# Kernel tuning notes

Measured on AMD Instinct MI355X. Metric: run time of the kernel, lower is better.

## Reference

```python
import jax, jax.numpy as jnp
import numpy as np

B, H, S, D = 4, 16, 2048, 64


def setup_inputs() -> dict:
    key = jax.random.key(0)
    kq, kk, kv = jax.random.split(key, 3)
    q = jax.random.normal(kq, (B, H, S, D), dtype=jnp.float32)
    k = jax.random.normal(kk, (B, H, S, D), dtype=jnp.float32)
    v = jax.random.normal(kv, (B, H, S, D), dtype=jnp.float32)
    # causal mask: 1 where position is masked (j > i), matching mask * -1e9 additive convention
    mask = jnp.triu(jnp.ones((S, S), dtype=jnp.float32), k=1)[None, None]  # [1,1,S,S]
    return {"q": q, "k": k, "v": v, "mask": mask}


def reference(q, k, v, mask):
    scale = 1.0 / jnp.sqrt(jnp.asarray(q.shape[-1], dtype=q.dtype))
    # [B,H,S,S] scores
    scores = jnp.einsum('bhqd,bhkd->bhqk', q, k) * scale
    scores = scores + mask * (-1e9)
    attn = jax.nn.softmax(scores, axis=-1)
    return jnp.einsum('bhqk,bhkd->bhqd', attn, v)
```

## Files before the change

### kernel.cpp

```cpp
#include <hip/hip_runtime.h>
#include <hip/hip_bf16.h>

namespace {

constexpr int Bc = 4, Hc = 16, Sc = 2048, Dc = 64;

using bf16x2 = __attribute__((ext_vector_type(2))) __bf16;
using bf16x8 = __attribute__((ext_vector_type(8))) __bf16;
using f32x4  = __attribute__((ext_vector_type(4))) float;
using f32x16 = __attribute__((ext_vector_type(16))) float;
using uint4v = __attribute__((ext_vector_type(4))) unsigned int;

__device__ __forceinline__ float exp2_hw(float x) {
#if __has_builtin(__builtin_amdgcn_exp2f)
  return __builtin_amdgcn_exp2f(x);
#else
  return exp2f(x);
#endif
}

__device__ __forceinline__ unsigned pk_bf16(float a, float b) {
  bf16x2 t = { (__bf16)a, (__bf16)b };
  return __builtin_bit_cast(unsigned, t);
}

__device__ __forceinline__ void pl32swap(unsigned& a, unsigned& b) {
  asm volatile("s_nop 1\n\tv_permlane32_swap_b32 %0, %1\n\ts_nop 1"
               : "+v"(a), "+v"(b));
}
__device__ __forceinline__ void xhalf_pair(float x, float& lo, float& hi) {
  unsigned a, b;
  asm volatile("v_mov_b32 %0, %2\n\t"
               "v_mov_b32 %1, %2\n\t"
               "s_nop 1\n\t"
               "v_permlane32_swap_b32 %0, %1\n\t"
               "s_nop 1"
               : "=&v"(a), "=&v"(b)
               : "v"(x));
  lo = __builtin_bit_cast(float, a);
  hi = __builtin_bit_cast(float, b);
}
__device__ __forceinline__ float xhalf_sum(float x) {
  float lo, hi; xhalf_pair(x, lo, hi); return lo + hi;
}

__device__ __forceinline__ int vswz(int d) { return ((d >> 4) ^ d) & 7; }

__global__ __launch_bounds__(256, 2)
void fattn_kernel(const float* __restrict__ Q, const float* __restrict__ K,
                  const float* __restrict__ V, float* __restrict__ O) {
  const int tid  = threadIdx.x;
  const int wid  = tid >> 6;
  const int lane = tid & 63;
  const int l31  = lane & 31;
  const int hi   = lane >> 5;

  const int flat = blockIdx.x + 8 * blockIdx.y;
  const int w    = (flat & 7) * 64 + (flat >> 3);
  const int p    = w & 7;
  const int bh   = w >> 3;

  const size_t base = (size_t)bh * (Sc * Dc);
  const float* Qb = Q + base;
  const float* Kb = K + base;
  const float* Vb = V + base;
  float*       Ob = O + base;

  __shared__ __align__(16) __bf16 k_lds[3][64][64];
  __shared__ __align__(16) __bf16 vt_lds[3][64][64];

  const int srow = tid >> 2;
  const int scol = (tid & 3) * 16;
  const int ssw  = (srow & 7) << 3;

  constexpr float QSC = 0.125f * 1.44269504088896f;

  for (int half = 0; half < 2; ++half) {
    const int qp = half ? (15 - p) : p;
    const int qb = qp * 128;
    const int wq = qb + wid * 32;
    const int nkb = 2 * qp + 2;
    const int tl  = 2 * qp + (wid >> 1);

    bf16x8 qf[4];
    {
      const float* qrow = Qb + (size_t)(wq + l31) * Dc;
      #pragma unroll
      for (int s = 0; s < 4; ++s) {
        const float* src = qrow + s * 16 + hi * 8;
        f32x4 a0 = *(const f32x4*)src;
        f32x4 a1 = *(const f32x4*)(src + 4);
        uint4v wv;
        wv[0] = pk_bf16(a0[0] * QSC, a0[1] * QSC);
        wv[1] = pk_bf16(a0[2] * QSC, a0[3] * QSC);
        wv[2] = pk_bf16(a1[0] * QSC, a1[1] * QSC);
        wv[3] = pk_bf16(a1[2] * QSC, a1[3] * QSC);
        qf[s] = __builtin_bit_cast(bf16x8, wv);
      }
    }

    f32x16 o0, o1;
    #pragma unroll
    for (int i = 0; i < 16; ++i) { o0[i] = 0.f; o1[i] = 0.f; }
    float l = 0.f;
    bf16x8 pfp0, pfp1, pfp2, pfp3;

    {
      const float* ksrc = Kb + (size_t)srow * Dc + scol;
      f32x4 a0 = *(const f32x4*)ksrc;
      f32x4 a1 = *(const f32x4*)(ksrc + 4);
      f32x4 a2 = *(const f32x4*)(ksrc + 8);
      f32x4 a3 = *(const f32x4*)(ksrc + 12);
      const float* vsrc = Vb + (size_t)srow * Dc + scol;
      f32x4 b0 = *(const f32x4*)vsrc;
      f32x4 b1 = *(const f32x4*)(vsrc + 4);
      f32x4 b2 = *(const f32x4*)(vsrc + 8);
      f32x4 b3 = *(const f32x4*)(vsrc + 12);
      uint4v w0, w1;
      w0[0] = pk_bf16(a0[0], a0[1]); w0[1] = pk_bf16(a0[2], a0[3]);
      w0[2] = pk_bf16(a1[0], a1[1]); w0[3] = pk_bf16(a1[2], a1[3]);
      w1[0] = pk_bf16(a2[0], a2[1]); w1[1] = pk_bf16(a2[2], a2[3]);
      w1[2] = pk_bf16(a3[0], a3[1]); w1[3] = pk_bf16(a3[2], a3[3]);
      *(uint4v*)&k_lds[0][srow][scol ^ ssw]       = w0;
      *(uint4v*)&k_lds[0][srow][(scol + 8) ^ ssw] = w1;
      f32x4 bb[4] = { b0, b1, b2, b3 };
      #pragma unroll
      for (int c = 0; c < 4; ++c)
        #pragma unroll
        for (int e = 0; e < 4; ++e) {
          const int dd = scol + 4 * c + e;
          vt_lds[0][dd][srow ^ (vswz(dd) << 3)] = (__bf16)bb[c][e];
        }
    }
    __syncthreads();

    int bq = 0;
    for (int t = 0; t <= nkb; ++t) {
      const int bp = (bq + 2 >= 3) ? bq - 1 : bq + 2;
      const int bw = (bq + 1 >= 3) ? bq - 2 : bq + 1;
      const int kbase = t * 64;
      const bool doQK = (t < nkb) && (t <= tl);
      const bool doPV = (t >= 1) && (t - 1 <= tl);
      const bool pre  = (t + 1 < nkb);

      f32x4 a0, a1, a2, a3, b0, b1, b2, b3;
      if (pre) {
        const float* ksrc = Kb + (size_t)(kbase + 64 + srow) * Dc + scol;
        a0 = *(const f32x4*)ksrc;
        a1 = *(const f32x4*)(ksrc + 4);
        a2 = *(const f32x4*)(ksrc + 8);
        a3 = *(const f32x4*)(ksrc + 12);
        const float* vsrc = Vb + (size_t)(kbase + 64 + srow) * Dc + scol;
        b0 = *(const f32x4*)vsrc;
        b1 = *(const f32x4*)(vsrc + 4);
        b2 = *(const f32x4*)(vsrc + 8);
        b3 = *(const f32x4*)(vsrc + 12);
      }

      f32x16 s0, s1;
      if (doQK) {
        #pragma unroll
        for (int i = 0; i < 16; ++i) { s0[i] = 0.f; s1[i] = 0.f; }
        const int ksw = (l31 & 7) << 3;
        __builtin_amdgcn_s_setprio(1);
        #pragma unroll
        for (int s = 0; s < 4; ++s) {
          bf16x8 kf = *(const bf16x8*)&k_lds[bq][l31][(s * 16 + hi * 8) ^ ksw];
          s0 = __builtin_amdgcn_mfma_f32_32x32x16_bf16(kf, qf[s], s0, 0, 0, 0);
        }
        #pragma unroll
        for (int s = 0; s < 4; ++s) {
          bf16x8 kf = *(const bf16x8*)&k_lds[bq][32 + l31][(s * 16 + hi * 8) ^ ksw];
          s1 = __builtin_amdgcn_mfma_f32_32x32x16_bf16(kf, qf[s], s1, 0, 0, 0);
        }
        __builtin_amdgcn_s_setprio(0);
      }

      if (doPV) {
        const int vd0 = l31, vd1 = 32 + l31;
        const int vs0 = vswz(vd0) << 3, vs1 = vswz(vd1) << 3;
        const __bf16 (*vc)[64] = vt_lds[bp];
        bf16x8 vf;
        __builtin_amdgcn_s_setprio(1);
        vf = *(const bf16x8*)&vc[vd0][(hi * 8) ^ vs0];
        o0 = __builtin_amdgcn_mfma_f32_32x32x16_bf16(vf, pfp0, o0, 0, 0, 0);
        vf = *(const bf16x8*)&vc[vd0][(16 + hi * 8) ^ vs0];
        o0 = __builtin_amdgcn_mfma_f32_32x32x16_bf16(vf, pfp1, o0, 0, 0, 0);
        vf = *(const bf16x8*)&vc[vd0][(32 + hi * 8) ^ vs0];
        o0 = __builtin_amdgcn_mfma_f32_32x32x16_bf16(vf, pfp2, o0, 0, 0, 0);
        vf = *(const bf16x8*)&vc[vd0][(48 + hi * 8) ^ vs0];
        o0 = __builtin_amdgcn_mfma_f32_32x32x16_bf16(vf, pfp3, o0, 0, 0, 0);
        vf = *(const bf16x8*)&vc[vd1][(hi * 8) ^ vs1];
        o1 = __builtin_amdgcn_mfma_f32_32x32x16_bf16(vf, pfp0, o1, 0, 0, 0);
        vf = *(const bf16x8*)&vc[vd1][(16 + hi * 8) ^ vs1];
        o1 = __builtin_amdgcn_mfma_f32_32x32x16_bf16(vf, pfp1, o1, 0, 0, 0);
        vf = *(const bf16x8*)&vc[vd1][(32 + hi * 8) ^ vs1];
        o1 = __builtin_amdgcn_mfma_f32_32x32x16_bf16(vf, pfp2, o1, 0, 0, 0);
        vf = *(const bf16x8*)&vc[vd1][(48 + hi * 8) ^ vs1];
        o1 = __builtin_amdgcn_mfma_f32_32x32x16_bf16(vf, pfp3, o1, 0, 0, 0);
        __builtin_amdgcn_s_setprio(0);
      }

      if (doQK) {
        if (kbase + 63 > wq) {
          const int q   = wq + l31;
          const int dq0 = q - (kbase + 4 * hi);
          const int dq1 = q - (kbase + 32 + 4 * hi);
          #pragma unroll
          for (int i = 0; i < 16; ++i) {
            const int off = (i & 3) + 8 * (i >> 2);
            if (off > dq0) s0[i] = -1e30f;
            if (off > dq1) s1[i] = -1e30f;
          }
        }
        #pragma unroll
        for (int i = 0; i < 16; ++i) {
          s0[i] = exp2_hw(s0[i]);
          s1[i] = exp2_hw(s1[i]);
        }
        float sm[16];
        #pragma unroll
        for (int i = 0; i < 16; ++i) sm[i] = s0[i] + s1[i];
        #pragma unroll
        for (int st = 8; st > 0; st >>= 1)
          #pragma unroll
          for (int i = 0; i < st; ++i) sm[i] += sm[i + st];
        l += xhalf_sum(sm[0]);

        uint4v wv;
        unsigned t0, t1, t2, t3;
        t0 = pk_bf16(s0[0], s0[1]);  t1 = pk_bf16(s0[2], s0[3]);
        t2 = pk_bf16(s0[4], s0[5]);  t3 = pk_bf16(s0[6], s0[7]);
        pl32swap(t0, t2); pl32swap(t1, t3);
        wv[0] = t0; wv[1] = t1; wv[2] = t2; wv[3] = t3;
        pfp0 = __builtin_bit_cast(bf16x8, wv);
        t0 = pk_bf16(s0[8], s0[9]);   t1 = pk_bf16(s0[10], s0[11]);
        t2 = pk_bf16(s0[12], s0[13]); t3 = pk_bf16(s0[14], s0[15]);
        pl32swap(t0, t2); pl32swap(t1, t3);
        wv[0] = t0; wv[1] = t1; wv[2] = t2; wv[3] = t3;
        pfp1 = __builtin_bit_cast(bf16x8, wv);
        t0 = pk_bf16(s1[0], s1[1]);  t1 = pk_bf16(s1[2], s1[3]);
        t2 = pk_bf16(s1[4], s1[5]);  t3 = pk_bf16(s1[6], s1[7]);
        pl32swap(t0, t2); pl32swap(t1, t3);
        wv[0] = t0; wv[1] = t1; wv[2] = t2; wv[3] = t3;
        pfp2 = __builtin_bit_cast(bf16x8, wv);
        t0 = pk_bf16(s1[8], s1[9]);   t1 = pk_bf16(s1[10], s1[11]);
        t2 = pk_bf16(s1[12], s1[13]); t3 = pk_bf16(s1[14], s1[15]);
        pl32swap(t0, t2); pl32swap(t1, t3);
        wv[0] = t0; wv[1] = t1; wv[2] = t2; wv[3] = t3;
        pfp3 = __builtin_bit_cast(bf16x8, wv);
      }

      if (pre) {
        uint4v w0, w1;
        w0[0] = pk_bf16(a0[0], a0[1]); w0[1] = pk_bf16(a0[2], a0[3]);
        w0[2] = pk_bf16(a1[0], a1[1]); w0[3] = pk_bf16(a1[2], a1[3]);
        w1[0] = pk_bf16(a2[0], a2[1]); w1[1] = pk_bf16(a2[2], a2[3]);
        w1[2] = pk_bf16(a3[0], a3[1]); w1[3] = pk_bf16(a3[2], a3[3]);
        *(uint4v*)&k_lds[bw][srow][scol ^ ssw]       = w0;
        *(uint4v*)&k_lds[bw][srow][(scol + 8) ^ ssw] = w1;
        f32x4 bb[4] = { b0, b1, b2, b3 };
        #pragma unroll
        for (int c = 0; c < 4; ++c)
          #pragma unroll
          for (int e = 0; e < 4; ++e) {
            const int dd = scol + 4 * c + e;
            vt_lds[bw][dd][srow ^ (vswz(dd) << 3)] = (__bf16)bb[c][e];
          }
      }
      if (t < nkb) __syncthreads();
      bq = bw;
    }

    const float inv = 1.0f / l;
    float* orow = Ob + (size_t)(wq + l31) * Dc;
    #pragma unroll
    for (int b = 0; b < 4; ++b) {
      f32x4 u0, u1;
      #pragma unroll
      for (int e = 0; e < 4; ++e) { u0[e] = o0[4 * b + e] * inv; u1[e] = o1[4 * b + e] * inv; }
      *(f32x4*)(orow + 8 * b + 4 * hi)      = u0;
      *(f32x4*)(orow + 32 + 8 * b + 4 * hi) = u1;
    }
    __syncthreads();
  }
}

}

extern "C" void kernel_launch(void* const* d_in, const int* in_sizes, int n_in,
                              void* d_out, int out_size, void* d_ws, size_t ws_size,
                              hipStream_t stream) {
  const float* q = (const float*)d_in[0];
  const float* k = (const float*)d_in[1];
  const float* v = (const float*)d_in[2];
  float* o = (float*)d_out;
  dim3 grid(8, Bc * Hc);
  fattn_kernel<<<grid, dim3(256), 0, stream>>>(q, k, v, o);
}
```

Measured before the change: 64.10 us.

## Deepen K/V global prefetch to two tiles ahead with ping-pong registers

Global loads of K/V tiles are now issued two iterations ahead into alternating register sets (A/B), with the loop unrolled by two through a macro so the register sets can swap statically. Conversion and LDS stores still happen one tile ahead. The goal is to hide more global memory latency behind the MFMA and softmax work. In exchange it uses about 32 more VGPRs, which may lower occupancy or cause spills.

```diff
diff --git a/kernel.cpp b/kernel.cpp
--- a/kernel.cpp
+++ b/kernel.cpp
@@ -74,6 +74,137 @@
   const int ssw  = (srow & 7) << 3;
 
   constexpr float QSC = 0.125f * 1.44269504088896f;
+
+#define BODY(T, SI, SW)                                                         \
+  {                                                                             \
+    const int kbase_ = (T) * 64;                                                \
+    const bool doQK_ = ((T) < nkb) && ((T) <= tl);                              \
+    const bool doPV_ = ((T) >= 1) && ((T) - 1 <= tl);                           \
+    const bool preL_ = ((T) + 2 < nkb);                                         \
+    const bool preW_ = ((T) + 1 < nkb);                                         \
+    const int bp_ = (bq + 2 >= 3) ? bq - 1 : bq + 2;                            \
+    const int bw_ = (bq + 1 >= 3) ? bq - 2 : bq + 1;                            \
+    if (preL_) {                                                                \
+      const float* ksrc_ = Kb + (size_t)(kbase_ + 128 + srow) * Dc + scol;      \
+      SI##k0 = *(const f32x4*)ksrc_;                                            \
+      SI##k1 = *(const f32x4*)(ksrc_ + 4);                                      \
+      SI##k2 = *(const f32x4*)(ksrc_ + 8);                                      \
+      SI##k3 = *(const f32x4*)(ksrc_ + 12);                                     \
+      const float* vsrc_ = Vb + (size_t)(kbase_ + 128 + srow) * Dc + scol;      \
+      SI##v0 = *(const f32x4*)vsrc_;                                            \
+      SI##v1 = *(const f32x4*)(vsrc_ + 4);                                      \
+      SI##v2 = *(const f32x4*)(vsrc_ + 8);                                      \
+      SI##v3 = *(const f32x4*)(vsrc_ + 12);                                     \
+    }                                                                           \
+    f32x16 s0_, s1_;                                                            \
+    if (doQK_) {                                                                \
+      _Pragma("unroll")                                                         \
+      for (int i = 0; i < 16; ++i) { s0_[i] = 0.f; s1_[i] = 0.f; }              \
+      const int ksw_ = (l31 & 7) << 3;                                          \
+      __builtin_amdgcn_s_setprio(1);                                            \
+      _Pragma("unroll")                                                         \
+      for (int s = 0; s < 4; ++s) {                                             \
+        bf16x8 kf_ = *(const bf16x8*)&k_lds[bq][l31][(s * 16 + hi * 8) ^ ksw_]; \
+        s0_ = __builtin_amdgcn_mfma_f32_32x32x16_bf16(kf_, qf[s], s0_, 0, 0, 0);\
+      }                                                                         \
+      _Pragma("unroll")                                                         \
+      for (int s = 0; s < 4; ++s) {                                             \
+        bf16x8 kf_ = *(const bf16x8*)&k_lds[bq][32 + l31][(s * 16 + hi * 8) ^ ksw_]; \
+        s1_ = __builtin_amdgcn_mfma_f32_32x32x16_bf16(kf_, qf[s], s1_, 0, 0, 0);\
+      }                                                                         \
+      __builtin_amdgcn_s_setprio(0);                                            \
+    }                                                                           \
+    if (doPV_) {                                                                \
+      const int vd0_ = l31, vd1_ = 32 + l31;                                    \
+      const int vs0_ = vswz(vd0_) << 3, vs1_ = vswz(vd1_) << 3;                 \
+      const __bf16 (*vc_)[64] = vt_lds[bp_];                                    \
+      bf16x8 vf_;                                                               \
+      __builtin_amdgcn_s_setprio(1);                                            \
+      vf_ = *(const bf16x8*)&vc_[vd0_][(hi * 8) ^ vs0_];                        \
+      o0 = __builtin_amdgcn_mfma_f32_32x32x16_bf16(vf_, pfp0, o0, 0, 0, 0);     \
+      vf_ = *(const bf16x8*)&vc_[vd0_][(16 + hi * 8) ^ vs0_];                   \
+      o0 = __builtin_amdgcn_mfma_f32_32x32x16_bf16(vf_, pfp1, o0, 0, 0, 0);     \
+      vf_ = *(const bf16x8*)&vc_[vd0_][(32 + hi * 8) ^ vs0_];                   \
+      o0 = __builtin_amdgcn_mfma_f32_32x32x16_bf16(vf_, pfp2, o0, 0, 0, 0);     \
+      vf_ = *(const bf16x8*)&vc_[vd0_][(48 + hi * 8) ^ vs0_];                   \
+      o0 = __builtin_amdgcn_mfma_f32_32x32x16_bf16(vf_, pfp3, o0, 0, 0, 0);     \
+      vf_ = *(const bf16x8*)&vc_[vd1_][(hi * 8) ^ vs1_];                        \
+      o1 = __builtin_amdgcn_mfma_f32_32x32x16_bf16(vf_, pfp0, o1, 0, 0, 0);     \
+      vf_ = *(const bf16x8*)&vc_[vd1_][(16 + hi * 8) ^ vs1_];                   \
+      o1 = __builtin_amdgcn_mfma_f32_32x32x16_bf16(vf_, pfp1, o1, 0, 0, 0);     \
+      vf_ = *(const bf16x8*)&vc_[vd1_][(32 + hi * 8) ^ vs1_];                   \
+      o1 = __builtin_amdgcn_mfma_f32_32x32x16_bf16(vf_, pfp2, o1, 0, 0, 0);     \
+      vf_ = *(const bf16x8*)&vc_[vd1_][(48 + hi * 8) ^ vs1_];                   \
+      o1 = __builtin_amdgcn_mfma_f32_32x32x16_bf16(vf_, pfp3, o1, 0, 0, 0);     \
+      __builtin_amdgcn_s_setprio(0);                                            \
+    }                                                                           \
+    if (doQK_) {                                                                \
+      if (kbase_ + 63 > wq) {                                                   \
+        const int q_   = wq + l31;                                              \
+        const int dq0_ = q_ - (kbase_ + 4 * hi);                                \
+        const int dq1_ = q_ - (kbase_ + 32 + 4 * hi);                           \
+        _Pragma("unroll")                                                       \
+        for (int i = 0; i < 16; ++i) {                                          \
+          const int off_ = (i & 3) + 8 * (i >> 2);                              \
+          if (off_ > dq0_) s0_[i] = -1e30f;                                     \
+          if (off_ > dq1_) s1_[i] = -1e30f;                                     \
+        }                                                                       \
+      }                                                                         \
+      _Pragma("unroll")                                                         \
+      for (int i = 0; i < 16; ++i) {                                            \
+        s0_[i] = exp2_hw(s0_[i]);                                               \
+        s1_[i] = exp2_hw(s1_[i]);                                               \
+      }                                                                         \
+      float sm_[16];                                                            \
+      _Pragma("unroll")                                                         \
+      for (int i = 0; i < 16; ++i) sm_[i] = s0_[i] + s1_[i];                    \
+      _Pragma("unroll")                                                         \
+      for (int st = 8; st > 0; st >>= 1)                                        \
+        _Pragma("unroll")                                                       \
+        for (int i = 0; i < st; ++i) sm_[i] += sm_[i + st];                     \
+      l += xhalf_sum(sm_[0]);                                                   \
+      uint4v wv_;                                                               \
+      unsigned t0_, t1_, t2_, t3_;                                              \
+      t0_ = pk_bf16(s0_[0], s0_[1]);  t1_ = pk_bf16(s0_[2], s0_[3]);            \
+      t2_ = pk_bf16(s0_[4], s0_[5]);  t3_ = pk_bf16(s0_[6], s0_[7]);            \
+      pl32swap(t0_, t2_); pl32swap(t1_, t3_);                                   \
+      wv_[0] = t0_; wv_[1] = t1_; wv_[2] = t2_; wv_[3] = t3_;                   \
+      pfp0 = __builtin_bit_cast(bf16x8, wv_);                                   \
+      t0_ = pk_bf16(s0_[8], s0_[9]);   t1_ = pk_bf16(s0_[10], s0_[11]);         \
+      t2_ = pk_bf16(s0_[12], s0_[13]); t3_ = pk_bf16(s0_[14], s0_[15]);         \
+      pl32swap(t0_, t2_); pl32swap(t1_, t3_);                                   \
+      wv_[0] = t0_; wv_[1] = t1_; wv_[2] = t2_; wv_[3] = t3_;                   \
+      pfp1 = __builtin_bit_cast(bf16x8, wv_);                                   \
+      t0_ = pk_bf16(s1_[0], s1_[1]);  t1_ = pk_bf16(s1_[2], s1_[3]);            \
+      t2_ = pk_bf16(s1_[4], s1_[5]);  t3_ = pk_bf16(s1_[6], s1_[7]);            \
+      pl32swap(t0_, t2_); pl32swap(t1_, t3_);                                   \
+      wv_[0] = t0_; wv_[1] = t1_; wv_[2] = t2_; wv_[3] = t3_;                   \
+      pfp2 = __builtin_bit_cast(bf16x8, wv_);                                   \
+      t0_ = pk_bf16(s1_[8], s1_[9]);   t1_ = pk_bf16(s1_[10], s1_[11]);         \
+      t2_ = pk_bf16(s1_[12], s1_[13]); t3_ = pk_bf16(s1_[14], s1_[15]);         \
+      pl32swap(t0_, t2_); pl32swap(t1_, t3_);                                   \
+      wv_[0] = t0_; wv_[1] = t1_; wv_[2] = t2_; wv_[3] = t3_;                   \
+      pfp3 = __builtin_bit_cast(bf16x8, wv_);                                   \
+    }                                                                           \
+    if (preW_) {                                                                \
+      uint4v w0_, w1_;                                                          \
+      w0_[0] = pk_bf16(SW##k0[0], SW##k0[1]); w0_[1] = pk_bf16(SW##k0[2], SW##k0[3]); \
+      w0_[2] = pk_bf16(SW##k1[0], SW##k1[1]); w0_[3] = pk_bf16(SW##k1[2], SW##k1[3]); \
+      w1_[0] = pk_bf16(SW##k2[0], SW##k2[1]); w1_[1] = pk_bf16(SW##k2[2], SW##k2[3]); \
+      w1_[2] = pk_bf16(SW##k3[0], SW##k3[1]); w1_[3] = pk_bf16(SW##k3[2], SW##k3[3]); \
+      *(uint4v*)&k_lds[bw_][srow][scol ^ ssw]       = w0_;                      \
+      *(uint4v*)&k_lds[bw_][srow][(scol + 8) ^ ssw] = w1_;                      \
+      _Pragma("unroll")                                                         \
+      for (int e = 0; e < 4; ++e) {                                             \
+        vt_lds[bw_][scol + e     ][srow ^ (vswz(scol + e     ) << 3)] = (__bf16)SW##v0[e]; \
+        vt_lds[bw_][scol + 4 + e ][srow ^ (vswz(scol + 4 + e ) << 3)] = (__bf16)SW##v1[e]; \
+        vt_lds[bw_][scol + 8 + e ][srow ^ (vswz(scol + 8 + e ) << 3)] = (__bf16)SW##v2[e]; \
+        vt_lds[bw_][scol + 12 + e][srow ^ (vswz(scol + 12 + e) << 3)] = (__bf16)SW##v3[e]; \
+      }                                                                         \
+    }                                                                           \
+    if ((T) < nkb) __syncthreads();                                             \
+    bq = bw_;                                                                   \
+  }
 
   for (int half = 0; half < 2; ++half) {
     const int qp = half ? (15 - p) : p;
@@ -105,6 +236,9 @@
     float l = 0.f;
     bf16x8 pfp0, pfp1, pfp2, pfp3;
 
+    f32x4 Ak0, Ak1, Ak2, Ak3, Av0, Av1, Av2, Av3;
+    f32x4 Bk0, Bk1, Bk2, Bk3, Bv0, Bv1, Bv2, Bv3;
+
     {
       const float* ksrc = Kb + (size_t)srow * Dc + scol;
       f32x4 a0 = *(const f32x4*)ksrc;
@@ -116,6 +250,17 @@
       f32x4 b1 = *(const f32x4*)(vsrc + 4);
       f32x4 b2 = *(const f32x4*)(vsrc + 8);
       f32x4 b3 = *(const f32x4*)(vsrc + 12);
+      const float* ksrc1 = Kb + (size_t)(64 + srow) * Dc + scol;
+      Bk0 = *(const f32x4*)ksrc1;
+      Bk1 = *(const f32x4*)(ksrc1 + 4);
+      Bk2 = *(const f32x4*)(ksrc1 + 8);
+      Bk3 = *(const f32x4*)(ksrc1 + 12);
+      const float* vsrc1 = Vb + (size_t)(64 + srow) * Dc + scol;
+      Bv0 = *(const f32x4*)vsrc1;
+      Bv1 = *(const f32x4*)(vsrc1 + 4);
+      Bv2 = *(const f32x4*)(vsrc1 + 8);
+      Bv3 = *(const f32x4*)(vsrc1 + 12);
+
       uint4v w0, w1;
       w0[0] = pk_bf16(a0[0], a0[1]); w0[1] = pk_bf16(a0[2], a0[3]);
       w0[2] = pk_bf16(a1[0], a1[1]); w0[3] = pk_bf16(a1[2], a1[3]);
@@ -135,141 +280,9 @@
     __syncthreads();
 
     int bq = 0;
-    for (int t = 0; t <= nkb; ++t) {
-      const int bp = (bq + 2 >= 3) ? bq - 1 : bq + 2;
-      const int bw = (bq + 1 >= 3) ? bq - 2 : bq + 1;
-      const int kbase = t * 64;
-      const bool doQK = (t < nkb) && (t <= tl);
-      const bool doPV = (t >= 1) && (t - 1 <= tl);
-      const bool pre  = (t + 1 < nkb);
-
-      f32x4 a0, a1, a2, a3, b0, b1, b2, b3;
-      if (pre) {
-        const float* ksrc = Kb + (size_t)(kbase + 64 + srow) * Dc + scol;
-        a0 = *(const f32x4*)ksrc;
-        a1 = *(const f32x4*)(ksrc + 4);
-        a2 = *(const f32x4*)(ksrc + 8);
-        a3 = *(const f32x4*)(ksrc + 12);
-        const float* vsrc = Vb + (size_t)(kbase + 64 + srow) * Dc + scol;
-        b0 = *(const f32x4*)vsrc;
-        b1 = *(const f32x4*)(vsrc + 4);
-        b2 = *(const f32x4*)(vsrc + 8);
-        b3 = *(const f32x4*)(vsrc + 12);
-      }
-
-      f32x16 s0, s1;
-      if (doQK) {
-        #pragma unroll
-        for (int i = 0; i < 16; ++i) { s0[i] = 0.f; s1[i] = 0.f; }
-        const int ksw = (l31 & 7) << 3;
-        __builtin_amdgcn_s_setprio(1);
-        #pragma unroll
-        for (int s = 0; s < 4; ++s) {
-          bf16x8 kf = *(const bf16x8*)&k_lds[bq][l31][(s * 16 + hi * 8) ^ ksw];
-          s0 = __builtin_amdgcn_mfma_f32_32x32x16_bf16(kf, qf[s], s0, 0, 0, 0);
-        }
-        #pragma unroll
-        for (int s = 0; s < 4; ++s) {
-          bf16x8 kf = *(const bf16x8*)&k_lds[bq][32 + l31][(s * 16 + hi * 8) ^ ksw];
-          s1 = __builtin_amdgcn_mfma_f32_32x32x16_bf16(kf, qf[s], s1, 0, 0, 0);
-        }
-        __builtin_amdgcn_s_setprio(0);
-      }
-
-      if (doPV) {
-        const int vd0 = l31, vd1 = 32 + l31;
-        const int vs0 = vswz(vd0) << 3, vs1 = vswz(vd1) << 3;
-        const __bf16 (*vc)[64] = vt_lds[bp];
-        bf16x8 vf;
-        __builtin_amdgcn_s_setprio(1);
-        vf = *(const bf16x8*)&vc[vd0][(hi * 8) ^ vs0];
-        o0 = __builtin_amdgcn_mfma_f32_32x32x16_bf16(vf, pfp0, o0, 0, 0, 0);
-        vf = *(const bf16x8*)&vc[vd0][(16 + hi * 8) ^ vs0];
-        o0 = __builtin_amdgcn_mfma_f32_32x32x16_bf16(vf, pfp1, o0, 0, 0, 0);
-        vf = *(const bf16x8*)&vc[vd0][(32 + hi * 8) ^ vs0];
-        o0 = __builtin_amdgcn_mfma_f32_32x32x16_bf16(vf, pfp2, o0, 0, 0, 0);
-        vf = *(const bf16x8*)&vc[vd0][(48 + hi * 8) ^ vs0];
-        o0 = __builtin_amdgcn_mfma_f32_32x32x16_bf16(vf, pfp3, o0, 0, 0, 0);
-        vf = *(const bf16x8*)&vc[vd1][(hi * 8) ^ vs1];
-        o1 = __builtin_amdgcn_mfma_f32_32x32x16_bf16(vf, pfp0, o1, 0, 0, 0);
-        vf = *(const bf16x8*)&vc[vd1][(16 + hi * 8) ^ vs1];
-        o1 = __builtin_amdgcn_mfma_f32_32x32x16_bf16(vf, pfp1, o1, 0, 0, 0);
-        vf = *(const bf16x8*)&vc[vd1][(32 + hi * 8) ^ vs1];
-        o1 = __builtin_amdgcn_mfma_f32_32x32x16_bf16(vf, pfp2, o1, 0, 0, 0);
-        vf = *(const bf16x8*)&vc[vd1][(48 + hi * 8) ^ vs1];
-        o1 = __builtin_amdgcn_mfma_f32_32x32x16_bf16(vf, pfp3, o1, 0, 0, 0);
-        __builtin_amdgcn_s_setprio(0);
-      }
-
-      if (doQK) {
-        if (kbase + 63 > wq) {
-          const int q   = wq + l31;
-          const int dq0 = q - (kbase + 4 * hi);
-          const int dq1 = q - (kbase + 32 + 4 * hi);
-          #pragma unroll
-          for (int i = 0; i < 16; ++i) {
-            const int off = (i & 3) + 8 * (i >> 2);
-            if (off > dq0) s0[i] = -1e30f;
-            if (off > dq1) s1[i] = -1e30f;
-          }
-        }
-        #pragma unroll
-        for (int i = 0; i < 16; ++i) {
-          s0[i] = exp2_hw(s0[i]);
-          s1[i] = exp2_hw(s1[i]);
-        }
-        float sm[16];
-        #pragma unroll
-        for (int i = 0; i < 16; ++i) sm[i] = s0[i] + s1[i];
-        #pragma unroll
-        for (int st = 8; st > 0; st >>= 1)
-          #pragma unroll
-          for (int i = 0; i < st; ++i) sm[i] += sm[i + st];
-        l += xhalf_sum(sm[0]);
-
-        uint4v wv;
-        unsigned t0, t1, t2, t3;
-        t0 = pk_bf16(s0[0], s0[1]);  t1 = pk_bf16(s0[2], s0[3]);
-        t2 = pk_bf16(s0[4], s0[5]);  t3 = pk_bf16(s0[6], s0[7]);
-        pl32swap(t0, t2); pl32swap(t1, t3);
-        wv[0] = t0; wv[1] = t1; wv[2] = t2; wv[3] = t3;
-        pfp0 = __builtin_bit_cast(bf16x8, wv);
-        t0 = pk_bf16(s0[8], s0[9]);   t1 = pk_bf16(s0[10], s0[11]);
-        t2 = pk_bf16(s0[12], s0[13]); t3 = pk_bf16(s0[14], s0[15]);
-        pl32swap(t0, t2); pl32swap(t1, t3);
-        wv[0] = t0; wv[1] = t1; wv[2] = t2; wv[3] = t3;
-        pfp1 = __builtin_bit_cast(bf16x8, wv);
-        t0 = pk_bf16(s1[0], s1[1]);  t1 = pk_bf16(s1[2], s1[3]);
-        t2 = pk_bf16(s1[4], s1[5]);  t3 = pk_bf16(s1[6], s1[7]);
-        pl32swap(t0, t2); pl32swap(t1, t3);
-        wv[0] = t0; wv[1] = t1; wv[2] = t2; wv[3] = t3;
-        pfp2 = __builtin_bit_cast(bf16x8, wv);
-        t0 = pk_bf16(s1[8], s1[9]);   t1 = pk_bf16(s1[10], s1[11]);
-        t2 = pk_bf16(s1[12], s1[13]); t3 = pk_bf16(s1[14], s1[15]);
-        pl32swap(t0, t2); pl32swap(t1, t3);
-        wv[0] = t0; wv[1] = t1; wv[2] = t2; wv[3] = t3;
-        pfp3 = __builtin_bit_cast(bf16x8, wv);
-      }
-
-      if (pre) {
-        uint4v w0, w1;
-        w0[0] = pk_bf16(a0[0], a0[1]); w0[1] = pk_bf16(a0[2], a0[3]);
-        w0[2] = pk_bf16(a1[0], a1[1]); w0[3] = pk_bf16(a1[2], a1[3]);
-        w1[0] = pk_bf16(a2[0], a2[1]); w1[1] = pk_bf16(a2[2], a2[3]);
-        w1[2] = pk_bf16(a3[0], a3[1]); w1[3] = pk_bf16(a3[2], a3[3]);
-        *(uint4v*)&k_lds[bw][srow][scol ^ ssw]       = w0;
-        *(uint4v*)&k_lds[bw][srow][(scol + 8) ^ ssw] = w1;
-        f32x4 bb[4] = { b0, b1, b2, b3 };
-        #pragma unroll
-        for (int c = 0; c < 4; ++c)
-          #pragma unroll
-          for (int e = 0; e < 4; ++e) {
-            const int dd = scol + 4 * c + e;
-            vt_lds[bw][dd][srow ^ (vswz(dd) << 3)] = (__bf16)bb[c][e];
-          }
-      }
-      if (t < nkb) __syncthreads();
-      bq = bw;
+    for (int t = 0; t <= nkb; t += 2) {
+      BODY(t, A, B);
+      if (t + 1 <= nkb) { BODY(t + 1, B, A); }
     }
 
     const float inv = 1.0f / l;
@@ -284,6 +297,7 @@
     }
     __syncthreads();
   }
+#undef BODY
 }
 
 }
```

After: 82.97 us. 29.5% more time.

## Deepen K/V prefetch to two tiles ahead with four-stage LDS ring

Applied to the files above, without the earlier changes.

Grows the K/V LDS ring from three to four stages and keeps the next-next tile's global loads in registers, so each global load has a full iteration to land before it is converted and stored. The LDS store for tile t+1 moves to the start of the iteration, and the trailing __syncthreads is replaced by an explicit lgkmcnt wait plus a single s_barrier before the QK compute. This is meant to hide global memory latency and cut one barrier per iteration. In exchange it uses more LDS and more live registers, which may lower occupancy.

```diff
diff --git a/kernel.cpp b/kernel.cpp
--- a/kernel.cpp
+++ b/kernel.cpp
@@ -66,8 +66,8 @@
   const float* Vb = V + base;
   float*       Ob = O + base;
 
-  __shared__ __align__(16) __bf16 k_lds[3][64][64];
-  __shared__ __align__(16) __bf16 vt_lds[3][64][64];
+  __shared__ __align__(16) __bf16 k_lds[4][64][64];
+  __shared__ __align__(16) __bf16 vt_lds[4][64][64];
 
   const int srow = tid >> 2;
   const int scol = (tid & 3) * 16;
@@ -104,6 +104,8 @@
     for (int i = 0; i < 16; ++i) { o0[i] = 0.f; o1[i] = 0.f; }
     float l = 0.f;
     bf16x8 pfp0, pfp1, pfp2, pfp3;
+
+    f32x4 Rk0, Rk1, Rk2, Rk3, Rv0, Rv1, Rv2, Rv3;
 
     {
       const float* ksrc = Kb + (size_t)srow * Dc + scol;
@@ -131,31 +133,58 @@
           const int dd = scol + 4 * c + e;
           vt_lds[0][dd][srow ^ (vswz(dd) << 3)] = (__bf16)bb[c][e];
         }
+      const float* ksrc1 = Kb + (size_t)(64 + srow) * Dc + scol;
+      Rk0 = *(const f32x4*)ksrc1;
+      Rk1 = *(const f32x4*)(ksrc1 + 4);
+      Rk2 = *(const f32x4*)(ksrc1 + 8);
+      Rk3 = *(const f32x4*)(ksrc1 + 12);
+      const float* vsrc1 = Vb + (size_t)(64 + srow) * Dc + scol;
+      Rv0 = *(const f32x4*)vsrc1;
+      Rv1 = *(const f32x4*)(vsrc1 + 4);
+      Rv2 = *(const f32x4*)(vsrc1 + 8);
+      Rv3 = *(const f32x4*)(vsrc1 + 12);
     }
-    __syncthreads();
-
-    int bq = 0;
+
     for (int t = 0; t <= nkb; ++t) {
-      const int bp = (bq + 2 >= 3) ? bq - 1 : bq + 2;
-      const int bw = (bq + 1 >= 3) ? bq - 2 : bq + 1;
+      const int bq = t & 3;
+      const int bp = (t - 1) & 3;
+      const int bw = (t + 1) & 3;
       const int kbase = t * 64;
       const bool doQK = (t < nkb) && (t <= tl);
       const bool doPV = (t >= 1) && (t - 1 <= tl);
-      const bool pre  = (t + 1 < nkb);
-
-      f32x4 a0, a1, a2, a3, b0, b1, b2, b3;
-      if (pre) {
-        const float* ksrc = Kb + (size_t)(kbase + 64 + srow) * Dc + scol;
-        a0 = *(const f32x4*)ksrc;
-        a1 = *(const f32x4*)(ksrc + 4);
-        a2 = *(const f32x4*)(ksrc + 8);
-        a3 = *(const f32x4*)(ksrc + 12);
-        const float* vsrc = Vb + (size_t)(kbase + 64 + srow) * Dc + scol;
-        b0 = *(const f32x4*)vsrc;
-        b1 = *(const f32x4*)(vsrc + 4);
-        b2 = *(const f32x4*)(vsrc + 8);
-        b3 = *(const f32x4*)(vsrc + 12);
-      }
+
+      if (t + 1 < nkb) {
+        uint4v w0, w1;
+        w0[0] = pk_bf16(Rk0[0], Rk0[1]); w0[1] = pk_bf16(Rk0[2], Rk0[3]);
+        w0[2] = pk_bf16(Rk1[0], Rk1[1]); w0[3] = pk_bf16(Rk1[2], Rk1[3]);
+        w1[0] = pk_bf16(Rk2[0], Rk2[1]); w1[1] = pk_bf16(Rk2[2], Rk2[3]);
+        w1[2] = pk_bf16(Rk3[0], Rk3[1]); w1[3] = pk_bf16(Rk3[2], Rk3[3]);
+        *(uint4v*)&k_lds[bw][srow][scol ^ ssw]       = w0;
+        *(uint4v*)&k_lds[bw][srow][(scol + 8) ^ ssw] = w1;
+        #pragma unroll
+        for (int e = 0; e < 4; ++e) {
+          vt_lds[bw][scol + e     ][srow ^ (vswz(scol + e     ) << 3)] = (__bf16)Rv0[e];
+          vt_lds[bw][scol + 4 + e ][srow ^ (vswz(scol + 4 + e ) << 3)] = (__bf16)Rv1[e];
+          vt_lds[bw][scol + 8 + e ][srow ^ (vswz(scol + 8 + e ) << 3)] = (__bf16)Rv2[e];
+          vt_lds[bw][scol + 12 + e][srow ^ (vswz(scol + 12 + e) << 3)] = (__bf16)Rv3[e];
+        }
+      }
+
+      if (t + 2 < nkb) {
+        const float* ksrc = Kb + (size_t)(kbase + 128 + srow) * Dc + scol;
+        Rk0 = *(const f32x4*)ksrc;
+        Rk1 = *(const f32x4*)(ksrc + 4);
+        Rk2 = *(const f32x4*)(ksrc + 8);
+        Rk3 = *(const f32x4*)(ksrc + 12);
+        const float* vsrc = Vb + (size_t)(kbase + 128 + srow) * Dc + scol;
+        Rv0 = *(const f32x4*)vsrc;
+        Rv1 = *(const f32x4*)(vsrc + 4);
+        Rv2 = *(const f32x4*)(vsrc + 8);
+        Rv3 = *(const f32x4*)(vsrc + 12);
+      }
+
+      asm volatile("s_waitcnt lgkmcnt(0)" ::: "memory");
+      __builtin_amdgcn_s_barrier();
 
       f32x16 s0, s1;
       if (doQK) {
@@ -250,26 +279,6 @@
         wv[0] = t0; wv[1] = t1; wv[2] = t2; wv[3] = t3;
         pfp3 = __builtin_bit_cast(bf16x8, wv);
       }
-
-      if (pre) {
-        uint4v w0, w1;
-        w0[0] = pk_bf16(a0[0], a0[1]); w0[1] = pk_bf16(a0[2], a0[3]);
-        w0[2] = pk_bf16(a1[0], a1[1]); w0[3] = pk_bf16(a1[2], a1[3]);
-        w1[0] = pk_bf16(a2[0], a2[1]); w1[1] = pk_bf16(a2[2], a2[3]);
-        w1[2] = pk_bf16(a3[0], a3[1]); w1[3] = pk_bf16(a3[2], a3[3]);
-        *(uint4v*)&k_lds[bw][srow][scol ^ ssw]       = w0;
-        *(uint4v*)&k_lds[bw][srow][(scol + 8) ^ ssw] = w1;
-        f32x4 bb[4] = { b0, b1, b2, b3 };
-        #pragma unroll
-        for (int c = 0; c < 4; ++c)
-          #pragma unroll
-          for (int e = 0; e < 4; ++e) {
-            const int dd = scol + 4 * c + e;
-            vt_lds[bw][dd][srow ^ (vswz(dd) << 3)] = (__bf16)bb[c][e];
-          }
-      }
-      if (t < nkb) __syncthreads();
-      bq = bw;
     }
 
     const float inv = 1.0f / l;
```

After: 75.22 us. 17.4% more time.
